# Optimization experiments

Hardware: AMD Instinct MI355X
Metric: run time of the kernel (lower is better)

## Reference

```python
import jax, jax.numpy as jnp
import numpy as np

B, H, W, DIM, HEADS, WS, SHIFT, MLP_RATIO = 32, 56, 56, 256, 8, 7, 3, 4
N = WS * WS                      # tokens per window = 49
NW = (H // WS) * (W // WS)       # windows per image = 64
HEAD_DIM = DIM // HEADS
HIDDEN = DIM * MLP_RATIO


def _rel_index():
    # standard Swin relative position index, shape (N, N), values in [0, (2*WS-1)^2)
    coords = np.stack(np.meshgrid(np.arange(WS), np.arange(WS), indexing='ij')).reshape(2, -1)
    rel = (coords[:, :, None] - coords[:, None, :]).transpose(1, 2, 0)
    rel[:, :, 0] += WS - 1
    rel[:, :, 1] += WS - 1
    rel[:, :, 0] *= 2 * WS - 1
    return rel.sum(-1).astype(np.int32)


def _attn_mask():
    # shifted-window attention mask, shape (NW, N, N), values in {0, -100}
    img = np.zeros((H, W))
    slices = (slice(0, -WS), slice(-WS, -SHIFT), slice(-SHIFT, None))
    cnt = 0
    for hs in slices:
        for ws_ in slices:
            img[hs, ws_] = cnt
            cnt += 1
    mw = img.reshape(H // WS, WS, W // WS, WS).transpose(0, 2, 1, 3).reshape(-1, N)
    diff = mw[:, None, :] - mw[:, :, None]
    return np.where(diff != 0, -100.0, 0.0).astype(np.float32)


def setup_inputs() -> dict:
    key = jax.random.key(0)
    ks = jax.random.split(key, 16)
    s = 0.02
    return {
        'x': jax.random.normal(ks[0], (B, H * W, DIM), jnp.float32),
        'norm1_w': jnp.ones((DIM,), jnp.float32),
        'norm1_b': jnp.zeros((DIM,), jnp.float32),
        'qkv_w': jax.random.normal(ks[1], (3 * DIM, DIM), jnp.float32) * s,
        'qkv_b': jnp.zeros((3 * DIM,), jnp.float32),
        'rpb_table': jax.random.normal(ks[2], ((2 * WS - 1) ** 2, HEADS), jnp.float32) * s,
        'proj_w': jax.random.normal(ks[3], (DIM, DIM), jnp.float32) * s,
        'proj_b': jnp.zeros((DIM,), jnp.float32),
        'norm2_w': jnp.ones((DIM,), jnp.float32),
        'norm2_b': jnp.zeros((DIM,), jnp.float32),
        'fc1_w': jax.random.normal(ks[4], (HIDDEN, DIM), jnp.float32) * s,
        'fc1_b': jnp.zeros((HIDDEN,), jnp.float32),
        'fc2_w': jax.random.normal(ks[5], (DIM, HIDDEN), jnp.float32) * s,
        'fc2_b': jnp.zeros((DIM,), jnp.float32),
        'rel_idx': jnp.asarray(_rel_index()),
        'attn_mask': jnp.asarray(_attn_mask()),
    }


def _ln(t, w, b):
    mu = t.mean(-1, keepdims=True)
    var = ((t - mu) ** 2).mean(-1, keepdims=True)
    return (t - mu) * jax.lax.rsqrt(var + 1e-5) * w + b


def reference(x, norm1_w, norm1_b, qkv_w, qkv_b, rpb_table, proj_w, proj_b,
              norm2_w, norm2_b, fc1_w, fc1_b, fc2_w, fc2_b, rel_idx, attn_mask):
    Bz = x.shape[0]
    shortcut = x
    h = _ln(x, norm1_w, norm1_b).reshape(Bz, H, W, DIM)
    h = jnp.roll(h, (-SHIFT, -SHIFT), axis=(1, 2))                      # cyclic shift
    # window partition -> (Bz*NW, N, C)
    h = h.reshape(Bz, H // WS, WS, W // WS, WS, DIM).transpose(0, 1, 3, 2, 4, 5).reshape(-1, N, DIM)
    qkv = (h @ qkv_w.T + qkv_b).reshape(-1, N, 3, HEADS, HEAD_DIM).transpose(2, 0, 3, 1, 4)
    q, k, v = qkv[0], qkv[1], qkv[2]                                    # (Bz*NW, heads, N, d)
    scale = HEAD_DIM ** -0.5
    attn = jnp.einsum('whnd,whmd->whnm', q * scale, k)
    bias = rpb_table[rel_idx].transpose(2, 0, 1)                        # (heads, N, N)
    attn = attn + bias[None]
    attn = attn.reshape(Bz, NW, HEADS, N, N) + attn_mask[None, :, None]  # shift mask
    attn = jax.nn.softmax(attn.reshape(-1, HEADS, N, N), axis=-1)
    out = jnp.einsum('whnm,whmd->whnd', attn, v).transpose(0, 2, 1, 3).reshape(-1, N, DIM)
    out = out @ proj_w.T + proj_b
    # window reverse + un-shift
    out = out.reshape(Bz, H // WS, W // WS, WS, WS, DIM).transpose(0, 1, 3, 2, 4, 5).reshape(Bz, H, W, DIM)
    out = jnp.roll(out, (SHIFT, SHIFT), axis=(1, 2)).reshape(Bz, H * W, DIM)
    x = shortcut + out
    # residual MLP (pre-LN), exact GELU as in nn.GELU default
    h2 = _ln(x, norm2_w, norm2_b)
    h2 = jax.nn.gelu(h2 @ fc1_w.T + fc1_b, approximate=False)
    return x + (h2 @ fc2_w.T + fc2_b)
```

## Files before the change

### kernel.cpp

```cpp
#include <hip/hip_runtime.h>

typedef unsigned short ushort_t;
typedef __attribute__((ext_vector_type(8))) __bf16 bf16x8;
typedef __attribute__((ext_vector_type(4))) float floatx4;

#define TOKS 100352

__device__ __forceinline__ ushort_t f2bf(float f) {
    union { float f; unsigned u; } a; a.f = f;
    unsigned r = a.u + 0x7fffu + ((a.u >> 16) & 1u);
    return (ushort_t)(r >> 16);
}
__device__ __forceinline__ float bf2f(ushort_t u) {
    union { unsigned v; float f; } a; a.v = ((unsigned)u) << 16; return a.f;
}

__device__ __forceinline__ void async16(const void* g, void* l) {
    __builtin_amdgcn_global_load_lds(
        (const __attribute__((address_space(1))) unsigned int*)g,
        (__attribute__((address_space(3))) unsigned int*)l,
        16, 0, 0);
}

__device__ __forceinline__ int win_to_orig(int t) {
    int b = t / 3136, rr = t - b * 3136;
    int w_ = rr / 49, pos = rr - w_ * 49;
    int wi = w_ >> 3, wj = w_ & 7;
    int ti = pos / 7, tj = pos - ti * 7;
    int h = wi * 7 + ti + 3; if (h >= 56) h -= 56;
    int w = wj * 7 + tj + 3; if (w >= 56) w -= 56;
    return b * 3136 + h * 56 + w;
}

__global__ void convert_kernel(const float* __restrict__ qkv_w, const float* __restrict__ proj_w,
                               const float* __restrict__ fc1_w, const float* __restrict__ fc2_w,
                               const float* __restrict__ rpb, const int* __restrict__ rel_idx,
                               const float* __restrict__ amask, const float* __restrict__ qkv_b,
                               ushort_t* __restrict__ wq, ushort_t* __restrict__ wp,
                               ushort_t* __restrict__ w1, ushort_t* __restrict__ w2,
                               float* __restrict__ bmF, float* __restrict__ qb2) {
    const float scale = 0.17677669529663687f;
    int i = blockIdx.x * 256 + threadIdx.x;
    if (i < 196608) { float v = qkv_w[i]; wq[i] = f2bf(i < 65536 ? v * scale : v); }
    if (i < 65536)  wp[i] = f2bf(proj_w[i]);
    if (i < 262144) { w1[i] = f2bf(fc1_w[i]); w2[i] = f2bf(fc2_w[i]); }
    if (i < 768)    qb2[i] = qkv_b[i] * (i < 256 ? scale : 1.f);
    if (i < 2097152) {
        int r = i & 3, lane = (i >> 2) & 63, t = (i >> 8) & 15, wh = i >> 12;
        int head = wh & 7, wimg = wh >> 3;
        int mi = t >> 2, nj = t & 3;
        int quad = lane >> 4, l15 = lane & 15;
        int ii = mi * 16 + quad * 4 + r, jj = nj * 16 + l15;
        float val = -1e30f;
        if (ii < 49 && jj < 49)
            val = rpb[rel_idx[ii * 49 + jj] * 8 + head] + amask[wimg * 2401 + ii * 49 + jj];
        bmF[i] = val;
    }
}

__global__ __launch_bounds__(256) void ln_kernel(const float* __restrict__ xin,
                                                 const float* __restrict__ gw,
                                                 const float* __restrict__ gb,
                                                 ushort_t* __restrict__ outb) {
    const int wid = threadIdx.x >> 6, lane = threadIdx.x & 63;
    const int t_out = blockIdx.x * 4 + wid;
    const int t_in = win_to_orig(t_out);
    const float4* src = (const float4*)(xin + (long)t_in * 256);
    float4 v = src[lane];
    float s  = v.x + v.y + v.z + v.w;
    float s2 = v.x*v.x + v.y*v.y + v.z*v.z + v.w*v.w;
    #pragma unroll
    for (int d = 32; d >= 1; d >>= 1) { s += __shfl_xor(s, d, 64); s2 += __shfl_xor(s2, d, 64); }
    float mu  = s * 0.00390625f;
    float var = s2 * 0.00390625f - mu * mu;
    float ry  = rsqrtf(var + 1e-5f);
    float4 w4 = ((const float4*)gw)[lane], b4 = ((const float4*)gb)[lane];
    unsigned long long p =
          (unsigned long long)f2bf((v.x - mu) * ry * w4.x + b4.x)
        | ((unsigned long long)f2bf((v.y - mu) * ry * w4.y + b4.y) << 16)
        | ((unsigned long long)f2bf((v.z - mu) * ry * w4.z + b4.z) << 32)
        | ((unsigned long long)f2bf((v.w - mu) * ry * w4.w + b4.w) << 48);
    ((unsigned long long*)(outb + (long)t_out * 256))[lane] = p;
}

template <int MODE, int N_LD, int KD, int CT>
__global__ __launch_bounds__(256, 2) void gemm_kernel(const ushort_t* __restrict__ A,
                                                      const ushort_t* __restrict__ Bw,
                                                      const float* __restrict__ bias,
                                                      void* __restrict__ outp,
                                                      const ushort_t* __restrict__ x1w,
                                                      int rowOff) {
    __shared__ __align__(16) ushort_t As[128 * 32];
    __shared__ __align__(16) ushort_t Bs[128 * 32];
    const int tid = threadIdx.x;
    const int lane = tid & 63;
    const int wid = tid >> 6;
    const int wm = wid & 1, wn = wid >> 1;
    const int l15 = lane & 15, quad = lane >> 4;
    const int v = blockIdx.x;
    const int j = v >> 3;
    const long tileM = (long)((j / CT) * 8 + (v & 7)) * 128;
    const long tileN = (long)(j % CT) * 128;

    floatx4 acc[4][4];
    #pragma unroll
    for (int i = 0; i < 4; i++)
        #pragma unroll
        for (int jj = 0; jj < 4; jj++) acc[i][jj] = {0.f, 0.f, 0.f, 0.f};

    const int o1 = tid * 16;
    const int r1 = o1 >> 6, c1 = (o1 & 63) >> 1;
    const ushort_t* Ar1 = A + (tileM + r1) * KD + c1;
    const ushort_t* Ar2 = A + (tileM + r1 + 64) * KD + c1;
    const ushort_t* Br1 = Bw + (tileN + r1) * KD + c1;
    const ushort_t* Br2 = Bw + (tileN + r1 + 64) * KD + c1;
    ushort_t* Ad1 = &As[o1 >> 1];
    ushort_t* Ad2 = &As[(o1 >> 1) + 2048];
    ushort_t* Bd1 = &Bs[o1 >> 1];
    ushort_t* Bd2 = &Bs[(o1 >> 1) + 2048];

    for (int k0 = 0; k0 < KD; k0 += 32) {
        async16(Ar1 + k0, Ad1);
        async16(Ar2 + k0, Ad2);
        async16(Br1 + k0, Bd1);
        async16(Br2 + k0, Bd2);
        __syncthreads();
        bf16x8 af[4], bfr[4];
        #pragma unroll
        for (int mi = 0; mi < 4; mi++)
            af[mi] = *(const bf16x8*)&As[(wm * 64 + mi * 16 + l15) * 32 + quad * 8];
        #pragma unroll
        for (int nj = 0; nj < 4; nj++)
            bfr[nj] = *(const bf16x8*)&Bs[(wn * 64 + nj * 16 + l15) * 32 + quad * 8];
        #pragma unroll
        for (int mi = 0; mi < 4; mi++)
            #pragma unroll
            for (int nj = 0; nj < 4; nj++)
                acc[mi][nj] = __builtin_amdgcn_mfma_f32_16x16x32_bf16(af[mi], bfr[nj], acc[mi][nj], 0, 0, 0);
        __syncthreads();
    }

    #pragma unroll
    for (int mi = 0; mi < 4; mi++)
      #pragma unroll
      for (int nj = 0; nj < 4; nj++)
        #pragma unroll
        for (int r = 0; r < 4; r++) {
            long row = tileM + wm * 64 + mi * 16 + quad * 4 + r;
            long col = tileN + wn * 64 + nj * 16 + l15;
            float val = acc[mi][nj][r] + bias[col];
            if (MODE == 0) {
                ((ushort_t*)outp)[row * N_LD + col] = f2bf(val);
            } else if (MODE == 2) {
                float g = 0.5f * val * (1.f + erff(val * 0.70710678118654752f));
                ((ushort_t*)outp)[row * N_LD + col] = f2bf(g);
            } else {
                float res = bf2f(x1w[row * 256 + col]);
                int orig = win_to_orig((int)row + rowOff);
                ((float*)outp)[(long)orig * 256 + col] = val + res;
            }
        }
}

__global__ __launch_bounds__(256, 2) void proj_ln_kernel(
        const ushort_t* __restrict__ A, const ushort_t* __restrict__ Bw,
        const float* __restrict__ pb, const float* __restrict__ x_res,
        const float* __restrict__ n2w, const float* __restrict__ n2b,
        ushort_t* __restrict__ x1w, ushort_t* __restrict__ h2out) {
    __shared__ __align__(16) ushort_t As[64 * 32];
    __shared__ __align__(16) ushort_t Bs[256 * 32];
    __shared__ float red_s[4][64];
    __shared__ float red_q[4][64];
    const int tid = threadIdx.x, lane = tid & 63, wid = tid >> 6;
    const int l15 = lane & 15, quad = lane >> 4;
    const long tileM = (long)blockIdx.x * 64;

    floatx4 acc[4][4];
    #pragma unroll
    for (int i = 0; i < 4; i++)
        #pragma unroll
        for (int j = 0; j < 4; j++) acc[i][j] = {0.f, 0.f, 0.f, 0.f};

    const int oA = tid * 16;
    const int rA = oA >> 6, cA = (oA & 63) >> 1;
    const ushort_t* Ap = A + (tileM + rA) * 256 + cA;
    ushort_t* Ad = &As[oA >> 1];

    for (int k0 = 0; k0 < 256; k0 += 32) {
        async16(Ap + k0, Ad);
        #pragma unroll
        for (int ch = 0; ch < 4; ch++) {
            int o = ch * 4096 + oA;
            async16(Bw + (o >> 6) * 256 + ((o & 63) >> 1) + k0, &Bs[o >> 1]);
        }
        __syncthreads();
        bf16x8 af[4], bfr[4];
        #pragma unroll
        for (int mi = 0; mi < 4; mi++)
            af[mi] = *(const bf16x8*)&As[(mi * 16 + l15) * 32 + quad * 8];
        #pragma unroll
        for (int nj = 0; nj < 4; nj++)
            bfr[nj] = *(const bf16x8*)&Bs[(wid * 64 + nj * 16 + l15) * 32 + quad * 8];
        #pragma unroll
        for (int mi = 0; mi < 4; mi++)
            #pragma unroll
            for (int nj = 0; nj < 4; nj++)
                acc[mi][nj] = __builtin_amdgcn_mfma_f32_16x16x32_bf16(af[mi], bfr[nj], acc[mi][nj], 0, 0, 0);
        __syncthreads();
    }

    #pragma unroll
    for (int mi = 0; mi < 4; mi++)
      #pragma unroll
      for (int r = 0; r < 4; r++) {
        int iloc = mi * 16 + quad * 4 + r;
        int orig = win_to_orig((int)tileM + iloc);
        float s = 0.f, q = 0.f;
        #pragma unroll
        for (int nj = 0; nj < 4; nj++) {
            int col = wid * 64 + nj * 16 + l15;
            float val = acc[mi][nj][r] + pb[col] + x_res[(long)orig * 256 + col];
            x1w[(tileM + iloc) * 256 + col] = f2bf(val);
            acc[mi][nj][r] = val;
            s += val; q += val * val;
        }
        #pragma unroll
        for (int d = 1; d < 16; d <<= 1) { s += __shfl_xor(s, d, 64); q += __shfl_xor(q, d, 64); }
        if (l15 == 0) { red_s[wid][iloc] = s; red_q[wid][iloc] = q; }
      }
    __syncthreads();
    #pragma unroll
    for (int mi = 0; mi < 4; mi++)
      #pragma unroll
      for (int r = 0; r < 4; r++) {
        int iloc = mi * 16 + quad * 4 + r;
        float s = red_s[0][iloc] + red_s[1][iloc] + red_s[2][iloc] + red_s[3][iloc];
        float q = red_q[0][iloc] + red_q[1][iloc] + red_q[2][iloc] + red_q[3][iloc];
        float mu = s * 0.00390625f;
        float var = q * 0.00390625f - mu * mu;
        float rstd = rsqrtf(var + 1e-5f);
        #pragma unroll
        for (int nj = 0; nj < 4; nj++) {
            int col = wid * 64 + nj * 16 + l15;
            float val = acc[mi][nj][r];
            h2out[(tileM + iloc) * 256 + col] = f2bf((val - mu) * rstd * n2w[col] + n2b[col]);
        }
      }
}

__global__ __launch_bounds__(256) void attn_kernel(const ushort_t* __restrict__ qkv,
                                                   const float* __restrict__ bmF,
                                                   ushort_t* __restrict__ attnout) {
    __shared__ __align__(16) ushort_t lds[4 * 5832];
    const int tid = threadIdx.x, lane = tid & 63, wid = tid >> 6;
    ushort_t* Pl = &lds[wid * 5832];
    ushort_t* Vt = Pl + 49 * 72;
    const int whid = blockIdx.x * 4 + wid;
    const int win = whid >> 3, head = whid & 7;
    const int l15 = lane & 15, quad = lane >> 4;
    const long base = (long)win * 49 * 768;

    const floatx4* bmc = (const floatx4*)bmF
                       + ((long)((win & 63) * 8 + head) * 16) * 64 + lane;
    floatx4 S[4][4];
    #pragma unroll
    for (int mi = 0; mi < 4; mi++)
        #pragma unroll
        for (int nj = 0; nj < 4; nj++)
            S[mi][nj] = bmc[(mi * 4 + nj) * 64];

    bf16x8 qf[4], kf[4];
    #pragma unroll
    for (int t4 = 0; t4 < 4; t4++) {
        int tok = t4 * 16 + l15; if (tok > 48) tok = 48;
        const ushort_t* p = qkv + base + (long)tok * 768 + head * 32 + quad * 8;
        qf[t4] = *(const bf16x8*)p;
        kf[t4] = *(const bf16x8*)(p + 256);
    }

    const int jl = lane;
    const int jc = jl < 49 ? jl : 48;
    const uint4* vsrc = (const uint4*)(qkv + base + (long)jc * 768 + 512 + head * 32);
    uint4 vz; vz.x = vz.y = vz.z = vz.w = 0u;
    uint4 vv[4];
    #pragma unroll
    for (int q4 = 0; q4 < 4; q4++) vv[q4] = (jl < 49) ? vsrc[q4] : vz;

    #pragma unroll
    for (int mi = 0; mi < 4; mi++)
        #pragma unroll
        for (int nj = 0; nj < 4; nj++)
            S[mi][nj] = __builtin_amdgcn_mfma_f32_16x16x32_bf16(qf[mi], kf[nj], S[mi][nj], 0, 0, 0);

    #pragma unroll
    for (int q4 = 0; q4 < 4; q4++) {
        int db = q4 * 8;
        uint4 v4 = vv[q4];
        Vt[(db+0)*72 + jl] = (ushort_t)v4.x;  Vt[(db+1)*72 + jl] = (ushort_t)(v4.x >> 16);
        Vt[(db+2)*72 + jl] = (ushort_t)v4.y;  Vt[(db+3)*72 + jl] = (ushort_t)(v4.y >> 16);
        Vt[(db+4)*72 + jl] = (ushort_t)v4.z;  Vt[(db+5)*72 + jl] = (ushort_t)(v4.z >> 16);
        Vt[(db+6)*72 + jl] = (ushort_t)v4.w;  Vt[(db+7)*72 + jl] = (ushort_t)(v4.w >> 16);
    }

    float rinv[4][4];
    #pragma unroll
    for (int mi = 0; mi < 4; mi++)
      #pragma unroll
      for (int r = 0; r < 4; r++) {
          float m = fmaxf(fmaxf(S[mi][0][r], S[mi][1][r]), fmaxf(S[mi][2][r], S[mi][3][r]));
          #pragma unroll
          for (int d = 1; d < 16; d <<= 1) m = fmaxf(m, __shfl_xor(m, d, 64));
          float e[4], sum = 0.f;
          #pragma unroll
          for (int nj = 0; nj < 4; nj++) { e[nj] = __expf(S[mi][nj][r] - m); sum += e[nj]; }
          #pragma unroll
          for (int d = 1; d < 16; d <<= 1) sum += __shfl_xor(sum, d, 64);
          rinv[mi][r] = 1.f / sum;
          int i = mi * 16 + quad * 4 + r;
          if (i < 49) {
              #pragma unroll
              for (int nj = 0; nj < 4; nj++) Pl[i * 72 + (nj * 16 + l15)] = f2bf(e[nj]);
          }
      }


    floatx4 O[4][2];
    #pragma unroll
    for (int mi = 0; mi < 4; mi++) { O[mi][0] = {0.f,0.f,0.f,0.f}; O[mi][1] = {0.f,0.f,0.f,0.f}; }
    #pragma unroll
    for (int kc = 0; kc < 2; kc++) {
        bf16x8 pf[4], vf[2];
        #pragma unroll
        for (int mi = 0; mi < 4; mi++) {
            int pr = mi * 16 + l15; if (pr > 48) pr = 48;
            pf[mi] = *(const bf16x8*)&Pl[pr * 72 + kc * 32 + quad * 8];
        }
        #pragma unroll
        for (int n2 = 0; n2 < 2; n2++)
            vf[n2] = *(const bf16x8*)&Vt[(n2 * 16 + l15) * 72 + kc * 32 + quad * 8];
        #pragma unroll
        for (int mi = 0; mi < 4; mi++)
            #pragma unroll
            for (int n2 = 0; n2 < 2; n2++)
                O[mi][n2] = __builtin_amdgcn_mfma_f32_16x16x32_bf16(pf[mi], vf[n2], O[mi][n2], 0, 0, 0);
    }

    #pragma unroll
    for (int mi = 0; mi < 4; mi++)
      #pragma unroll
      for (int n2 = 0; n2 < 2; n2++)
        #pragma unroll
        for (int r = 0; r < 4; r++) {
            int i = mi * 16 + quad * 4 + r;
            if (i < 49) {
                long orow = ((long)win * 49 + i) * 256 + head * 32 + n2 * 16 + l15;
                attnout[orow] = f2bf(O[mi][n2][r] * rinv[mi][r]);
            }
        }
}

extern "C" void kernel_launch(void* const* d_in, const int* in_sizes, int n_in,
                              void* d_out, int out_size, void* d_ws, size_t ws_size,
                              hipStream_t stream) {
    const float* x      = (const float*)d_in[0];
    const float* n1w    = (const float*)d_in[1];
    const float* n1b    = (const float*)d_in[2];
    const float* qkv_w  = (const float*)d_in[3];
    const float* qkv_b  = (const float*)d_in[4];
    const float* rpb    = (const float*)d_in[5];
    const float* proj_w = (const float*)d_in[6];
    const float* proj_b = (const float*)d_in[7];
    const float* n2w    = (const float*)d_in[8];
    const float* n2b    = (const float*)d_in[9];
    const float* fc1_w  = (const float*)d_in[10];
    const float* fc1_b  = (const float*)d_in[11];
    const float* fc2_w  = (const float*)d_in[12];
    const float* fc2_b  = (const float*)d_in[13];
    const int*   rel_idx= (const int*)d_in[14];
    const float* amask  = (const float*)d_in[15];

    char* ws = (char*)d_ws;
    ushort_t* wq   = (ushort_t*)(ws + 0);
    ushort_t* wp   = (ushort_t*)(ws + 393216);
    ushort_t* w1   = (ushort_t*)(ws + 524288);
    ushort_t* w2   = (ushort_t*)(ws + 1048576);
    ushort_t* hwin = (ushort_t*)(ws + 1572864);
    ushort_t* qkvb = (ushort_t*)(ws + 52953088);
    ushort_t* h2   = (ushort_t*)(ws + 104333312);
    ushort_t* x1w  = (ushort_t*)(ws + 155713536);
    ushort_t* h3   = hwin;
    float* bmF = (float*)d_out;
    float* qb2 = (float*)((char*)d_out + 8388608);

    convert_kernel<<<8192, 256, 0, stream>>>(qkv_w, proj_w, fc1_w, fc2_w, rpb, rel_idx,
                                             amask, qkv_b, wq, wp, w1, w2, bmF, qb2);
    ln_kernel<<<TOKS / 4, 256, 0, stream>>>(x, n1w, n1b, hwin);
    gemm_kernel<0, 768, 256, 6><<<4704, 256, 0, stream>>>(hwin, wq, qb2, qkvb, nullptr, 0);
    attn_kernel<<<4096, 256, 0, stream>>>(qkvb, bmF, hwin);
    proj_ln_kernel<<<1568, 256, 0, stream>>>(hwin, wp, proj_b, x, n2w, n2b, x1w, h2);
    for (int c = 0; c < 2; c++) {
        gemm_kernel<2, 1024, 256, 8><<<3136, 256, 0, stream>>>(
            h2 + (long)c * 50176 * 256, w1, fc1_b, h3, nullptr, 0);
        gemm_kernel<4, 256, 1024, 2><<<784, 256, 0, stream>>>(
            h3, w2, fc2_b, (float*)d_out, x1w + (long)c * 50176 * 256, c * 50176);
    }
    (void)in_sizes; (void)n_in; (void)out_size; (void)ws_size;
}
```

Baseline: 640.3 us.

## Double-buffer LDS tiles in GEMM and proj-LN kernels to overlap loads with MFMA

Converts the K-loop of the generic GEMM kernel and the projection+LayerNorm kernel to a two-stage LDS ping-pong. The next K-slice is fetched with async global-to-LDS loads while the current one feeds the MFMAs, and explicit vmcnt waits plus raw s_barrier replace the full __syncthreads. This is meant to hide global load latency that the single-buffered loop exposed at every iteration. In exchange it doubles LDS use per block, which may lower occupancy, and the correctness of the hand-written vmcnt counts depends on the compiler's instruction ordering.

```diff
diff --git a/kernel.cpp b/kernel.cpp
--- a/kernel.cpp
+++ b/kernel.cpp
@@ -90,8 +90,8 @@
                                                       void* __restrict__ outp,
                                                       const ushort_t* __restrict__ x1w,
                                                       int rowOff) {
-    __shared__ __align__(16) ushort_t As[128 * 32];
-    __shared__ __align__(16) ushort_t Bs[128 * 32];
+    __shared__ __align__(16) ushort_t As[2][128 * 32];
+    __shared__ __align__(16) ushort_t Bs[2][128 * 32];
     const int tid = threadIdx.x;
     const int lane = tid & 63;
     const int wid = tid >> 6;
@@ -110,34 +110,45 @@
 
     const int o1 = tid * 16;
     const int r1 = o1 >> 6, c1 = (o1 & 63) >> 1;
+    const int lo = o1 >> 1;
     const ushort_t* Ar1 = A + (tileM + r1) * KD + c1;
     const ushort_t* Ar2 = A + (tileM + r1 + 64) * KD + c1;
     const ushort_t* Br1 = Bw + (tileN + r1) * KD + c1;
     const ushort_t* Br2 = Bw + (tileN + r1 + 64) * KD + c1;
-    ushort_t* Ad1 = &As[o1 >> 1];
-    ushort_t* Ad2 = &As[(o1 >> 1) + 2048];
-    ushort_t* Bd1 = &Bs[o1 >> 1];
-    ushort_t* Bd2 = &Bs[(o1 >> 1) + 2048];
-
-    for (int k0 = 0; k0 < KD; k0 += 32) {
-        async16(Ar1 + k0, Ad1);
-        async16(Ar2 + k0, Ad2);
-        async16(Br1 + k0, Bd1);
-        async16(Br2 + k0, Bd2);
-        __syncthreads();
+
+    async16(Ar1, &As[0][lo]);
+    async16(Ar2, &As[0][lo + 2048]);
+    async16(Br1, &Bs[0][lo]);
+    async16(Br2, &Bs[0][lo + 2048]);
+
+    #pragma unroll
+    for (int it = 0; it < KD / 32; ++it) {
+        const int buf = it & 1, nbuf = buf ^ 1;
+        const int k0 = it * 32;
+        if (it + 1 < KD / 32) {
+            async16(Ar1 + k0 + 32, &As[nbuf][lo]);
+            async16(Ar2 + k0 + 32, &As[nbuf][lo + 2048]);
+            async16(Br1 + k0 + 32, &Bs[nbuf][lo]);
+            async16(Br2 + k0 + 32, &Bs[nbuf][lo + 2048]);
+            asm volatile("s_waitcnt vmcnt(4)" ::: "memory");
+        } else {
+            asm volatile("s_waitcnt vmcnt(0)" ::: "memory");
+        }
+        __builtin_amdgcn_s_barrier();
         bf16x8 af[4], bfr[4];
         #pragma unroll
         for (int mi = 0; mi < 4; mi++)
-            af[mi] = *(const bf16x8*)&As[(wm * 64 + mi * 16 + l15) * 32 + quad * 8];
+            af[mi] = *(const bf16x8*)&As[buf][(wm * 64 + mi * 16 + l15) * 32 + quad * 8];
         #pragma unroll
         for (int nj = 0; nj < 4; nj++)
-            bfr[nj] = *(const bf16x8*)&Bs[(wn * 64 + nj * 16 + l15) * 32 + quad * 8];
+            bfr[nj] = *(const bf16x8*)&Bs[buf][(wn * 64 + nj * 16 + l15) * 32 + quad * 8];
         #pragma unroll
         for (int mi = 0; mi < 4; mi++)
             #pragma unroll
             for (int nj = 0; nj < 4; nj++)
                 acc[mi][nj] = __builtin_amdgcn_mfma_f32_16x16x32_bf16(af[mi], bfr[nj], acc[mi][nj], 0, 0, 0);
-        __syncthreads();
+        __builtin_amdgcn_sched_barrier(0);
+        __builtin_amdgcn_s_barrier();
     }
 
     #pragma unroll
@@ -167,8 +178,8 @@
         const float* __restrict__ pb, const float* __restrict__ x_res,
         const float* __restrict__ n2w, const float* __restrict__ n2b,
         ushort_t* __restrict__ x1w, ushort_t* __restrict__ h2out) {
-    __shared__ __align__(16) ushort_t As[64 * 32];
-    __shared__ __align__(16) ushort_t Bs[256 * 32];
+    __shared__ __align__(16) ushort_t As[2][64 * 32];
+    __shared__ __align__(16) ushort_t Bs[2][256 * 32];
     __shared__ float red_s[4][64];
     __shared__ float red_q[4][64];
     const int tid = threadIdx.x, lane = tid & 63, wid = tid >> 6;
@@ -184,29 +195,44 @@
     const int oA = tid * 16;
     const int rA = oA >> 6, cA = (oA & 63) >> 1;
     const ushort_t* Ap = A + (tileM + rA) * 256 + cA;
-    ushort_t* Ad = &As[oA >> 1];
-
-    for (int k0 = 0; k0 < 256; k0 += 32) {
-        async16(Ap + k0, Ad);
-        #pragma unroll
-        for (int ch = 0; ch < 4; ch++) {
-            int o = ch * 4096 + oA;
-            async16(Bw + (o >> 6) * 256 + ((o & 63) >> 1) + k0, &Bs[o >> 1]);
-        }
-        __syncthreads();
+
+    async16(Ap, &As[0][oA >> 1]);
+    #pragma unroll
+    for (int ch = 0; ch < 4; ch++) {
+        int o = ch * 4096 + oA;
+        async16(Bw + (o >> 6) * 256 + ((o & 63) >> 1), &Bs[0][o >> 1]);
+    }
+
+    #pragma unroll
+    for (int it = 0; it < 8; ++it) {
+        const int buf = it & 1, nbuf = buf ^ 1;
+        const int k0 = it * 32;
+        if (it + 1 < 8) {
+            async16(Ap + k0 + 32, &As[nbuf][oA >> 1]);
+            #pragma unroll
+            for (int ch = 0; ch < 4; ch++) {
+                int o = ch * 4096 + oA;
+                async16(Bw + (o >> 6) * 256 + ((o & 63) >> 1) + k0 + 32, &Bs[nbuf][o >> 1]);
+            }
+            asm volatile("s_waitcnt vmcnt(5)" ::: "memory");
+        } else {
+            asm volatile("s_waitcnt vmcnt(0)" ::: "memory");
+        }
+        __builtin_amdgcn_s_barrier();
         bf16x8 af[4], bfr[4];
         #pragma unroll
         for (int mi = 0; mi < 4; mi++)
-            af[mi] = *(const bf16x8*)&As[(mi * 16 + l15) * 32 + quad * 8];
+            af[mi] = *(const bf16x8*)&As[buf][(mi * 16 + l15) * 32 + quad * 8];
         #pragma unroll
         for (int nj = 0; nj < 4; nj++)
-            bfr[nj] = *(const bf16x8*)&Bs[(wid * 64 + nj * 16 + l15) * 32 + quad * 8];
+            bfr[nj] = *(const bf16x8*)&Bs[buf][(wid * 64 + nj * 16 + l15) * 32 + quad * 8];
         #pragma unroll
         for (int mi = 0; mi < 4; mi++)
             #pragma unroll
             for (int nj = 0; nj < 4; nj++)
                 acc[mi][nj] = __builtin_amdgcn_mfma_f32_16x16x32_bf16(af[mi], bfr[nj], acc[mi][nj], 0, 0, 0);
-        __syncthreads();
+        __builtin_amdgcn_sched_barrier(0);
+        __builtin_amdgcn_s_barrier();
     }
 
     #pragma unroll
```

Result: faster. 623.6 us (-2.6%).

## Pre-swizzle weights into MFMA fragment order and load B directly from global

Applied to the files above, without the earlier changes.

The one-time convert kernel now writes the bf16 weight matrices in MFMA fragment order, so each lane can load its B operand with one contiguous 16-byte global read instead of staging it through LDS. The GEMM and proj+LN kernels keep only the A tile in LDS, now double-buffered so the next K slice loads while the current one is multiplied, and their launch-bounds occupancy hints are raised. This aims to cut LDS traffic and barrier stalls and to fit more blocks per CU. The cost is that each wave fetches B from global/L2 on its own, with no sharing through LDS.

```diff
diff --git a/kernel.cpp b/kernel.cpp
--- a/kernel.cpp
+++ b/kernel.cpp
@@ -30,6 +30,12 @@
     int h = wi * 7 + ti + 3; if (h >= 56) h -= 56;
     int w = wj * 7 + tj + 3; if (w >= 56) w -= 56;
     return b * 3136 + h * 56 + w;
+}
+
+__device__ __forceinline__ long fragOff(int row, int k, int NPH) {
+    int cN = row >> 7, wn = (row >> 6) & 1, nj = (row >> 4) & 3, l15 = row & 15;
+    int it = k >> 5, quad = (k >> 3) & 3, e = k & 7;
+    return ((long)((cN * NPH + it) * 8 + wn * 4 + nj) * 64 + quad * 16 + l15) * 8 + e;
 }
 
 __global__ void convert_kernel(const float* __restrict__ qkv_w, const float* __restrict__ proj_w,
@@ -41,10 +47,20 @@
                                float* __restrict__ bmF, float* __restrict__ qb2) {
     const float scale = 0.17677669529663687f;
     int i = blockIdx.x * 256 + threadIdx.x;
-    if (i < 196608) { float v = qkv_w[i]; wq[i] = f2bf(i < 65536 ? v * scale : v); }
-    if (i < 65536)  wp[i] = f2bf(proj_w[i]);
-    if (i < 262144) { w1[i] = f2bf(fc1_w[i]); w2[i] = f2bf(fc2_w[i]); }
-    if (i < 768)    qb2[i] = qkv_b[i] * (i < 256 ? scale : 1.f);
+    if (i < 196608) {
+        int row = i >> 8, k = i & 255;
+        float v = qkv_w[i];
+        wq[fragOff(row, k, 8)] = f2bf(row < 256 ? v * scale : v);
+    }
+    if (i < 65536) {
+        int row = i >> 8, k = i & 255;
+        wp[fragOff(row, k, 8)] = f2bf(proj_w[i]);
+    }
+    if (i < 262144) {
+        { int row = i >> 8, k = i & 255;  w1[fragOff(row, k, 8)]  = f2bf(fc1_w[i]); }
+        { int row = i >> 10, k = i & 1023; w2[fragOff(row, k, 32)] = f2bf(fc2_w[i]); }
+    }
+    if (i < 768) qb2[i] = qkv_b[i] * (i < 256 ? scale : 1.f);
     if (i < 2097152) {
         int r = i & 3, lane = (i >> 2) & 63, t = (i >> 8) & 15, wh = i >> 12;
         int head = wh & 7, wimg = wh >> 3;
@@ -84,14 +100,13 @@
 }
 
 template <int MODE, int N_LD, int KD, int CT>
-__global__ __launch_bounds__(256, 2) void gemm_kernel(const ushort_t* __restrict__ A,
+__global__ __launch_bounds__(256, 3) void gemm_kernel(const ushort_t* __restrict__ A,
                                                       const ushort_t* __restrict__ Bw,
                                                       const float* __restrict__ bias,
                                                       void* __restrict__ outp,
                                                       const ushort_t* __restrict__ x1w,
                                                       int rowOff) {
-    __shared__ __align__(16) ushort_t As[128 * 32];
-    __shared__ __align__(16) ushort_t Bs[128 * 32];
+    __shared__ __align__(16) ushort_t As[2][128 * 32];
     const int tid = threadIdx.x;
     const int lane = tid & 63;
     const int wid = tid >> 6;
@@ -100,7 +115,9 @@
     const int v = blockIdx.x;
     const int j = v >> 3;
     const long tileM = (long)((j / CT) * 8 + (v & 7)) * 128;
-    const long tileN = (long)(j % CT) * 128;
+    const int cN = j % CT;
+    const long tileN = (long)cN * 128;
+    constexpr int NPH = KD / 32;
 
     floatx4 acc[4][4];
     #pragma unroll
@@ -110,28 +127,30 @@
 
     const int o1 = tid * 16;
     const int r1 = o1 >> 6, c1 = (o1 & 63) >> 1;
+    const int lo = o1 >> 1;
     const ushort_t* Ar1 = A + (tileM + r1) * KD + c1;
     const ushort_t* Ar2 = A + (tileM + r1 + 64) * KD + c1;
-    const ushort_t* Br1 = Bw + (tileN + r1) * KD + c1;
-    const ushort_t* Br2 = Bw + (tileN + r1 + 64) * KD + c1;
-    ushort_t* Ad1 = &As[o1 >> 1];
-    ushort_t* Ad2 = &As[(o1 >> 1) + 2048];
-    ushort_t* Bd1 = &Bs[o1 >> 1];
-    ushort_t* Bd2 = &Bs[(o1 >> 1) + 2048];
-
-    for (int k0 = 0; k0 < KD; k0 += 32) {
-        async16(Ar1 + k0, Ad1);
-        async16(Ar2 + k0, Ad2);
-        async16(Br1 + k0, Bd1);
-        async16(Br2 + k0, Bd2);
-        __syncthreads();
-        bf16x8 af[4], bfr[4];
+    const ushort_t* Bf = Bw + ((long)(cN * NPH * 8 + wn * 4) * 64 + lane) * 8;
+
+    async16(Ar1, &As[0][lo]);
+    async16(Ar2, &As[0][lo + 2048]);
+    __syncthreads();
+
+    #pragma unroll
+    for (int it = 0; it < NPH; ++it) {
+        const int buf = it & 1;
+        if (it + 1 < NPH) {
+            async16(Ar1 + (it + 1) * 32, &As[buf ^ 1][lo]);
+            async16(Ar2 + (it + 1) * 32, &As[buf ^ 1][lo + 2048]);
+        }
+        bf16x8 bfr[4];
+        #pragma unroll
+        for (int nj = 0; nj < 4; nj++)
+            bfr[nj] = *(const bf16x8*)(Bf + it * 4096 + nj * 512);
+        bf16x8 af[4];
         #pragma unroll
         for (int mi = 0; mi < 4; mi++)
-            af[mi] = *(const bf16x8*)&As[(wm * 64 + mi * 16 + l15) * 32 + quad * 8];
-        #pragma unroll
-        for (int nj = 0; nj < 4; nj++)
-            bfr[nj] = *(const bf16x8*)&Bs[(wn * 64 + nj * 16 + l15) * 32 + quad * 8];
+            af[mi] = *(const bf16x8*)&As[buf][(wm * 64 + mi * 16 + l15) * 32 + quad * 8];
         #pragma unroll
         for (int mi = 0; mi < 4; mi++)
             #pragma unroll
@@ -162,13 +181,12 @@
         }
 }
 
-__global__ __launch_bounds__(256, 2) void proj_ln_kernel(
+__global__ __launch_bounds__(256, 4) void proj_ln_kernel(
         const ushort_t* __restrict__ A, const ushort_t* __restrict__ Bw,
         const float* __restrict__ pb, const float* __restrict__ x_res,
         const float* __restrict__ n2w, const float* __restrict__ n2b,
         ushort_t* __restrict__ x1w, ushort_t* __restrict__ h2out) {
-    __shared__ __align__(16) ushort_t As[64 * 32];
-    __shared__ __align__(16) ushort_t Bs[256 * 32];
+    __shared__ __align__(16) ushort_t As[2][64 * 32];
     __shared__ float red_s[4][64];
     __shared__ float red_q[4][64];
     const int tid = threadIdx.x, lane = tid & 63, wid = tid >> 6;
@@ -184,23 +202,24 @@
     const int oA = tid * 16;
     const int rA = oA >> 6, cA = (oA & 63) >> 1;
     const ushort_t* Ap = A + (tileM + rA) * 256 + cA;
-    ushort_t* Ad = &As[oA >> 1];
-
-    for (int k0 = 0; k0 < 256; k0 += 32) {
-        async16(Ap + k0, Ad);
-        #pragma unroll
-        for (int ch = 0; ch < 4; ch++) {
-            int o = ch * 4096 + oA;
-            async16(Bw + (o >> 6) * 256 + ((o & 63) >> 1) + k0, &Bs[o >> 1]);
-        }
-        __syncthreads();
-        bf16x8 af[4], bfr[4];
+    const ushort_t* Bf = Bw + ((long)(((wid >> 1) * 8) * 8 + (wid & 1) * 4) * 64 + lane) * 8;
+
+    async16(Ap, &As[0][oA >> 1]);
+    __syncthreads();
+
+    #pragma unroll
+    for (int it = 0; it < 8; ++it) {
+        const int buf = it & 1;
+        if (it + 1 < 8)
+            async16(Ap + (it + 1) * 32, &As[buf ^ 1][oA >> 1]);
+        bf16x8 bfr[4];
+        #pragma unroll
+        for (int nj = 0; nj < 4; nj++)
+            bfr[nj] = *(const bf16x8*)(Bf + it * 4096 + nj * 512);
+        bf16x8 af[4];
         #pragma unroll
         for (int mi = 0; mi < 4; mi++)
-            af[mi] = *(const bf16x8*)&As[(mi * 16 + l15) * 32 + quad * 8];
-        #pragma unroll
-        for (int nj = 0; nj < 4; nj++)
-            bfr[nj] = *(const bf16x8*)&Bs[(wid * 64 + nj * 16 + l15) * 32 + quad * 8];
+            af[mi] = *(const bf16x8*)&As[buf][(mi * 16 + l15) * 32 + quad * 8];
         #pragma unroll
         for (int mi = 0; mi < 4; mi++)
             #pragma unroll
```

Measured after the change: 663.6 us. +3.6%, slower.
